# Optimization experiments

Hardware: AMD Instinct MI355X
Metric: run time of the kernel (lower is better)

## Reference

```python
import jax, jax.numpy as jnp
import numpy as np

N = 30000          # mesh vertices
B = 5 * 16         # p_bins * t_bins geodesic patch bins
NEURONS = [16, 64, 64, 32]


def setup_inputs() -> dict:
    key = jax.random.key(0)
    ks = jax.random.split(key, 7)
    x = jax.random.normal(ks[0], (N, NEURONS[0]), dtype=jnp.float32)
    conn = jax.random.randint(ks[1], (N, B), 0, N)  # per-vertex per-bin source index
    s1 = 1.0 / np.sqrt(NEURONS[0])
    W1 = jax.random.uniform(ks[2], (NEURONS[0], NEURONS[1]), minval=-s1, maxval=s1, dtype=jnp.float32)
    s2 = 1.0 / np.sqrt(B * NEURONS[1])
    Wg1 = jax.random.uniform(ks[3], (B, NEURONS[1], NEURONS[2]), minval=-s2, maxval=s2, dtype=jnp.float32)
    b1 = jax.random.uniform(ks[4], (NEURONS[2],), minval=-s2, maxval=s2, dtype=jnp.float32)
    s3 = 1.0 / np.sqrt(B * NEURONS[2])
    Wg2 = jax.random.uniform(ks[5], (B, NEURONS[2], NEURONS[3]), minval=-s3, maxval=s3, dtype=jnp.float32)
    b2 = jax.random.uniform(ks[6], (NEURONS[3],), minval=-s3, maxval=s3, dtype=jnp.float32)
    return {"x": x, "W1": W1, "Wg1": Wg1, "b1": b1, "Wg2": Wg2, "b2": b2, "conn": conn}


def _geodesic(h, conn, Wg, b):
    # gather geodesic patch: [N, B, C_in], then per-bin contraction
    patches = h[conn]                               # irregular gather
    return jnp.einsum("nbi,bio->no", patches, Wg) + b


def reference(x, W1, Wg1, b1, Wg2, b2, conn):
    h = jax.nn.relu(x @ W1)                         # linear_1 (no bias, l_bias=False)
    h = jax.nn.relu(_geodesic(h, conn, Wg1, b1))    # GC_1 + relu
    res = _geodesic(h, conn, Wg2, b2)               # GC_2
    norm = jnp.linalg.norm(res, axis=-1, keepdims=True)
    return res / norm
```

## Files before the change

### kernel.cpp

```cpp
#include <hip/hip_runtime.h>
#include <stdint.h>
#include <stddef.h>


typedef __attribute__((ext_vector_type(8))) short bf16x8;
typedef __attribute__((ext_vector_type(4))) float f32x4;

#define BINS 80
#define SPLITK 4
#define BPC 20

static __device__ __forceinline__ unsigned short f2bf(float f) {
  union { float f; unsigned int u; } c; c.f = f;
  unsigned int u = c.u;
  return (unsigned short)((u + 0x7FFFu + ((u >> 16) & 1u)) >> 16);
}

__global__ __launch_bounds__(256) void k_lin1(const float* __restrict__ x,
                                              const float* __restrict__ W1,
                                              unsigned short* __restrict__ h1b, int n) {
  __shared__ float w1s[16 * 64];
  int tid = threadIdx.x;
  for (int i = tid; i < 16 * 64; i += 256) w1s[i] = W1[i];
  __syncthreads();
  int v = blockIdx.x * 256 + tid;
  if (v >= n) return;
  const float4* xp = (const float4*)(x + (size_t)v * 16);
  float4 x0 = xp[0], x1 = xp[1], x2 = xp[2], x3 = xp[3];
  float xr[16] = {x0.x, x0.y, x0.z, x0.w, x1.x, x1.y, x1.z, x1.w,
                  x2.x, x2.y, x2.z, x2.w, x3.x, x3.y, x3.z, x3.w};
  float acc[64];
#pragma unroll
  for (int o = 0; o < 64; ++o) acc[o] = 0.f;
#pragma unroll
  for (int i = 0; i < 16; ++i) {
    float xi = xr[i];
#pragma unroll
    for (int o = 0; o < 64; ++o) acc[o] = fmaf(xi, w1s[i * 64 + o], acc[o]);
  }
  unsigned short* hr = h1b + (size_t)v * 64;
#pragma unroll
  for (int o8 = 0; o8 < 8; ++o8) {
    bf16x8 pack;
#pragma unroll
    for (int j = 0; j < 8; ++j) pack[j] = (short)f2bf(fmaxf(acc[o8 * 8 + j], 0.f));
    *(bf16x8*)(hr + o8 * 8) = pack;
  }
}

__global__ __launch_bounds__(256) void k_wimg(const float* __restrict__ Wg,
                                              unsigned char* __restrict__ img,
                                              int O, int total) {
  int t = blockIdx.x * 256 + threadIdx.x;
  if (t >= total) return;
  int c = t & 7;
  int o = (t >> 3) % O;
  int b = t / (O * 8);
  int boff = (o * 128 + c * 16) ^ ((o & 7) << 4);
  bf16x8 pack;
#pragma unroll
  for (int j = 0; j < 8; ++j)
    pack[j] = (short)f2bf(Wg[(size_t)(b * 64 + c * 8 + j) * O + o]);
  *(bf16x8*)(img + (size_t)b * (O * 128) + boff) = pack;
}

template <int OT>
__global__ __launch_bounds__(256) void k_geo_sk(const unsigned short* __restrict__ hin,
                                                const unsigned char* __restrict__ wimg,
                                                const int* __restrict__ conn,
                                                float* __restrict__ part, int n) {
  constexpr int TILEB = OT * 16 * 128;
  __shared__ int conn_s[64 * (BPC + 1)];
  __shared__ alignas(16) unsigned char wg_s[2][TILEB];

  const int tid = threadIdx.x;
  const int lane = tid & 63;
  const int wave = tid >> 6;
  const int ln15 = lane & 15;
  const int lq = lane >> 4;
  const int v0 = blockIdx.x * 64;
  const int chunk = blockIdx.y;
  const int bin0 = chunk * BPC;

  for (int idx = tid; idx < 64 * BPC; idx += 256) {
    int v = idx / BPC;
    int c = idx - v * BPC;
    int vv = v0 + v;
    if (vv > n - 1) vv = n - 1;
    conn_s[v * (BPC + 1) + c] = conn[(size_t)vv * BINS + bin0 + c];
  }

  auto stage = [&](int bin, int buf) {
    const unsigned char* src = wimg + (size_t)bin * TILEB + wave * (TILEB / 4) + lane * 16;
    unsigned char* dst = &wg_s[buf][wave * (TILEB / 4)];
#pragma unroll
    for (int i = 0; i < TILEB / 4096; ++i) {
      __builtin_amdgcn_global_load_lds(
          (const __attribute__((address_space(1))) unsigned int*)(const void*)(src + i * 1024),
          (__attribute__((address_space(3))) unsigned int*)(void*)(dst + i * 1024),
          16, 0, 0);
    }
  };

  int boffs[OT][2];
#pragma unroll
  for (int ot = 0; ot < OT; ++ot)
#pragma unroll
    for (int s = 0; s < 2; ++s) {
      int o = ot * 16 + ln15;
      boffs[ot][s] = (o * 128 + s * 64 + lq * 16) ^ ((o & 7) << 4);
    }

  f32x4 acc[OT];
#pragma unroll
  for (int ot = 0; ot < OT; ++ot) acc[ot] = (f32x4){0.f, 0.f, 0.f, 0.f};

  stage(bin0, 0);
  __syncthreads();

  const int crow = (wave * 16 + ln15) * (BPC + 1);
  const int koff = lq * 8;

  bf16x8 a0, a1;
  {
    int cidx = conn_s[crow];
    const unsigned short* arow = hin + (size_t)cidx * 64 + koff;
    a0 = *(const bf16x8*)(arow);
    a1 = *(const bf16x8*)(arow + 32);
  }

  for (int cb = 0; cb < BPC; ++cb) {
    int cur = cb & 1;
    bf16x8 na0 = a0, na1 = a1;
    if (cb + 1 < BPC) {
      stage(bin0 + cb + 1, cur ^ 1);
      int nc = conn_s[crow + cb + 1];
      const unsigned short* arow = hin + (size_t)nc * 64 + koff;
      na0 = *(const bf16x8*)(arow);
      na1 = *(const bf16x8*)(arow + 32);
    }

    const unsigned char* wb = wg_s[cur];
#pragma unroll
    for (int ot = 0; ot < OT; ++ot) {
      bf16x8 b0 = *(const bf16x8*)(wb + boffs[ot][0]);
      bf16x8 b1 = *(const bf16x8*)(wb + boffs[ot][1]);
      acc[ot] = __builtin_amdgcn_mfma_f32_16x16x32_bf16(a0, b0, acc[ot], 0, 0, 0);
      acc[ot] = __builtin_amdgcn_mfma_f32_16x16x32_bf16(a1, b1, acc[ot], 0, 0, 0);
    }
    __syncthreads();
    a0 = na0; a1 = na1;
  }

  constexpr int O = OT * 16;
  float* pbase = part + (size_t)chunk * n * O;
#pragma unroll
  for (int ot = 0; ot < OT; ++ot) {
#pragma unroll
    for (int r = 0; r < 4; ++r) {
      int v = v0 + wave * 16 + lq * 4 + r;
      if (v < n) pbase[(size_t)v * O + ot * 16 + ln15] = acc[ot][r];
    }
  }
}

__global__ __launch_bounds__(256) void k_fin1(const float* __restrict__ part,
                                              const float* __restrict__ bias,
                                              unsigned short* __restrict__ out, int n) {
  int t = blockIdx.x * 256 + threadIdx.x;
  int total = n * 16;
  if (t >= total) return;
  int base = t * 4;
  int o = base & 63;
  size_t stride = (size_t)n * 64;
  const float* p = part + base;
  float4 s = *(const float4*)(p);
#pragma unroll
  for (int c = 1; c < SPLITK; ++c) {
    float4 q = *(const float4*)(p + c * stride);
    s.x += q.x; s.y += q.y; s.z += q.z; s.w += q.w;
  }
  float4 b4 = *(const float4*)(bias + o);
  ushort4 pack;
  pack.x = f2bf(fmaxf(s.x + b4.x, 0.f));
  pack.y = f2bf(fmaxf(s.y + b4.y, 0.f));
  pack.z = f2bf(fmaxf(s.z + b4.z, 0.f));
  pack.w = f2bf(fmaxf(s.w + b4.w, 0.f));
  *(ushort4*)(out + base) = pack;
}

__global__ __launch_bounds__(256) void k_fin2(const float* __restrict__ part,
                                              const float* __restrict__ bias,
                                              float* __restrict__ out, int n) {
  int v = blockIdx.x * 16 + (threadIdx.x >> 4);
  int o = threadIdx.x & 15;
  if (v >= n) return;
  size_t stride = (size_t)n * 32;
  const float* p = part + (size_t)v * 32 + o;
  float a = 0.f, b = 0.f;
#pragma unroll
  for (int c = 0; c < SPLITK; ++c) {
    a += p[c * stride];
    b += p[c * stride + 16];
  }
  a += bias[o];
  b += bias[o + 16];
  float ss = a * a + b * b;
  ss += __shfl_xor(ss, 1);
  ss += __shfl_xor(ss, 2);
  ss += __shfl_xor(ss, 4);
  ss += __shfl_xor(ss, 8);
  float inv = 1.0f / sqrtf(ss);
  out[(size_t)v * 32 + o] = a * inv;
  out[(size_t)v * 32 + 16 + o] = b * inv;
}

extern "C" void kernel_launch(void* const* d_in, const int* in_sizes, int n_in,
                              void* d_out, int out_size, void* d_ws, size_t ws_size,
                              hipStream_t stream) {
  const float* x   = (const float*)d_in[0];
  const float* W1  = (const float*)d_in[1];
  const float* Wg1 = (const float*)d_in[2];
  const float* b1  = (const float*)d_in[3];
  const float* Wg2 = (const float*)d_in[4];
  const float* b2  = (const float*)d_in[5];
  const int*  conn = (const int*)d_in[6];
  int n = in_sizes[0] / 16;

  unsigned char* ws = (unsigned char*)d_ws;
  size_t hb = ((size_t)n * 64 * 2 + 255) & ~(size_t)255;
  unsigned short* h1b = (unsigned short*)(ws);
  unsigned short* h2b = (unsigned short*)(ws + hb);
  unsigned char*  w1i = ws + 2 * hb;
  unsigned char*  w2i = ws + 2 * hb + 80 * 8192;
  float* part = (float*)(ws + 2 * hb + 80 * 8192 + 80 * 4096);

  k_wimg<<<(80 * 64 * 8 + 255) / 256, 256, 0, stream>>>(Wg1, w1i, 64, 80 * 64 * 8);
  k_wimg<<<(80 * 32 * 8 + 255) / 256, 256, 0, stream>>>(Wg2, w2i, 32, 80 * 32 * 8);
  k_lin1<<<(n + 255) / 256, 256, 0, stream>>>(x, W1, h1b, n);

  int gb = (n + 63) / 64;
  k_geo_sk<4><<<dim3(gb, SPLITK), 256, 0, stream>>>(h1b, w1i, conn, part, n);
  k_fin1<<<(n * 16 + 255) / 256, 256, 0, stream>>>(part, b1, h2b, n);
  k_geo_sk<2><<<dim3(gb, SPLITK), 256, 0, stream>>>(h2b, w2i, conn, part, n);
  k_fin2<<<(n + 15) / 16, 256, 0, stream>>>(part, b2, (float*)d_out, n);
}
```

Measured before the change: 140.4 us.

## Deepen geodesic gather pipeline with 128-row tiles and manual vmcnt waits

The geodesic split-K kernel now processes 128 vertices per block, with two 16-row M tiles per wave, so each staged weight tile is reused across twice as many rows. Gathers and weight staging are issued two bins ahead into a 4-deep LDS ring and 3-deep register buffers. Completion is tracked with explicit s_waitcnt vmcnt values and a raw s_barrier instead of __syncthreads each step. This trades more registers and LDS, plus half as many blocks, for more loads in flight and less weight traffic. It also depends on the hand-counted vmcnt matching the instructions the compiler actually emits.

Measured after the change: 136.7 us. -2.6%, faster.

```diff
diff --git a/kernel.cpp b/kernel.cpp
--- a/kernel.cpp
+++ b/kernel.cpp
@@ -9,11 +9,20 @@
 #define BINS 80
 #define SPLITK 4
 #define BPC 20
+#define MROWS 128
 
 static __device__ __forceinline__ unsigned short f2bf(float f) {
   union { float f; unsigned int u; } c; c.f = f;
   unsigned int u = c.u;
   return (unsigned short)((u + 0x7FFFu + ((u >> 16) & 1u)) >> 16);
+}
+
+template <int N> static __device__ __forceinline__ void wait_vmcnt() {
+  if constexpr (N == 12)      asm volatile("s_waitcnt vmcnt(12)" ::: "memory");
+  else if constexpr (N == 10) asm volatile("s_waitcnt vmcnt(10)" ::: "memory");
+  else if constexpr (N == 6)  asm volatile("s_waitcnt vmcnt(6)" ::: "memory");
+  else if constexpr (N == 5)  asm volatile("s_waitcnt vmcnt(5)" ::: "memory");
+  else                        asm volatile("s_waitcnt vmcnt(0)" ::: "memory");
 }
 
 __global__ __launch_bounds__(256) void k_lin1(const float* __restrict__ x,
@@ -65,24 +74,27 @@
 }
 
 template <int OT>
-__global__ __launch_bounds__(256) void k_geo_sk(const unsigned short* __restrict__ hin,
-                                                const unsigned char* __restrict__ wimg,
-                                                const int* __restrict__ conn,
-                                                float* __restrict__ part, int n) {
+__global__ __launch_bounds__(256, 3) void k_geo_sk(const unsigned short* __restrict__ hin,
+                                                   const unsigned char* __restrict__ wimg,
+                                                   const int* __restrict__ conn,
+                                                   float* __restrict__ part, int n) {
   constexpr int TILEB = OT * 16 * 128;
-  __shared__ int conn_s[64 * (BPC + 1)];
-  __shared__ alignas(16) unsigned char wg_s[2][TILEB];
+  constexpr int SINSTS = TILEB / 4096;
+  constexpr int IPI = 4 + SINSTS;
+
+  __shared__ int conn_s[MROWS * (BPC + 1)];
+  __shared__ alignas(16) unsigned char wg_s[4][TILEB];
 
   const int tid = threadIdx.x;
   const int lane = tid & 63;
   const int wave = tid >> 6;
   const int ln15 = lane & 15;
   const int lq = lane >> 4;
-  const int v0 = blockIdx.x * 64;
+  const int v0 = blockIdx.x * MROWS;
   const int chunk = blockIdx.y;
   const int bin0 = chunk * BPC;
 
-  for (int idx = tid; idx < 64 * BPC; idx += 256) {
+  for (int idx = tid; idx < MROWS * BPC; idx += 256) {
     int v = idx / BPC;
     int c = idx - v * BPC;
     int vv = v0 + v;
@@ -90,78 +102,85 @@
     conn_s[v * (BPC + 1) + c] = conn[(size_t)vv * BINS + bin0 + c];
   }
 
-  auto stage = [&](int bin, int buf) {
-    const unsigned char* src = wimg + (size_t)bin * TILEB + wave * (TILEB / 4) + lane * 16;
-    unsigned char* dst = &wg_s[buf][wave * (TILEB / 4)];
-#pragma unroll
-    for (int i = 0; i < TILEB / 4096; ++i) {
+  int boffs[OT][2];
+#pragma unroll
+  for (int ot = 0; ot < OT; ++ot)
+#pragma unroll
+    for (int s = 0; s < 2; ++s) {
+      int o = ot * 16 + ln15;
+      boffs[ot][s] = (o * 128 + s * 64 + lq * 16) ^ ((o & 7) << 4);
+    }
+
+  const int koff = lq * 8;
+  bf16x8 As[3][2][2];
+  f32x4 acc[2][OT];
+#pragma unroll
+  for (int mt = 0; mt < 2; ++mt)
+#pragma unroll
+    for (int ot = 0; ot < OT; ++ot) acc[mt][ot] = (f32x4){0.f, 0.f, 0.f, 0.f};
+
+  auto issue = [&](int j) {
+#pragma unroll
+    for (int mt = 0; mt < 2; ++mt) {
+      int cidx = conn_s[(wave * 32 + mt * 16 + ln15) * (BPC + 1) + j];
+      const unsigned short* arow = hin + (size_t)cidx * 64 + koff;
+      As[j % 3][mt][0] = *(const bf16x8*)(arow);
+      As[j % 3][mt][1] = *(const bf16x8*)(arow + 32);
+    }
+    __builtin_amdgcn_sched_barrier(0);
+    const unsigned char* src =
+        wimg + (size_t)(bin0 + j) * TILEB + wave * (TILEB / 4) + lane * 16;
+    unsigned char* dst = &wg_s[j & 3][wave * (TILEB / 4)];
+#pragma unroll
+    for (int i = 0; i < SINSTS; ++i) {
       __builtin_amdgcn_global_load_lds(
           (const __attribute__((address_space(1))) unsigned int*)(const void*)(src + i * 1024),
           (__attribute__((address_space(3))) unsigned int*)(void*)(dst + i * 1024),
           16, 0, 0);
     }
+    __builtin_amdgcn_sched_barrier(0);
   };
 
-  int boffs[OT][2];
-#pragma unroll
-  for (int ot = 0; ot < OT; ++ot)
-#pragma unroll
-    for (int s = 0; s < 2; ++s) {
-      int o = ot * 16 + ln15;
-      boffs[ot][s] = (o * 128 + s * 64 + lq * 16) ^ ((o & 7) << 4);
-    }
-
-  f32x4 acc[OT];
-#pragma unroll
-  for (int ot = 0; ot < OT; ++ot) acc[ot] = (f32x4){0.f, 0.f, 0.f, 0.f};
-
-  stage(bin0, 0);
   __syncthreads();
-
-  const int crow = (wave * 16 + ln15) * (BPC + 1);
-  const int koff = lq * 8;
-
-  bf16x8 a0, a1;
-  {
-    int cidx = conn_s[crow];
-    const unsigned short* arow = hin + (size_t)cidx * 64 + koff;
-    a0 = *(const bf16x8*)(arow);
-    a1 = *(const bf16x8*)(arow + 32);
-  }
-
+  issue(0);
+  issue(1);
+
+#pragma unroll
   for (int cb = 0; cb < BPC; ++cb) {
-    int cur = cb & 1;
-    bf16x8 na0 = a0, na1 = a1;
-    if (cb + 1 < BPC) {
-      stage(bin0 + cb + 1, cur ^ 1);
-      int nc = conn_s[crow + cb + 1];
-      const unsigned short* arow = hin + (size_t)nc * 64 + koff;
-      na0 = *(const bf16x8*)(arow);
-      na1 = *(const bf16x8*)(arow + 32);
-    }
-
-    const unsigned char* wb = wg_s[cur];
+    if (cb + 2 < BPC) issue(cb + 2);
+    const int nafter = IPI * ((cb + 1 < BPC ? 1 : 0) + (cb + 2 < BPC ? 1 : 0));
+    if (nafter == 2 * IPI)      wait_vmcnt<2 * IPI>();
+    else if (nafter == IPI)     wait_vmcnt<IPI>();
+    else                        wait_vmcnt<0>();
+    __builtin_amdgcn_s_barrier();
+    __builtin_amdgcn_sched_barrier(0);
+
+    const unsigned char* wb = wg_s[cb & 3];
 #pragma unroll
     for (int ot = 0; ot < OT; ++ot) {
       bf16x8 b0 = *(const bf16x8*)(wb + boffs[ot][0]);
       bf16x8 b1 = *(const bf16x8*)(wb + boffs[ot][1]);
-      acc[ot] = __builtin_amdgcn_mfma_f32_16x16x32_bf16(a0, b0, acc[ot], 0, 0, 0);
-      acc[ot] = __builtin_amdgcn_mfma_f32_16x16x32_bf16(a1, b1, acc[ot], 0, 0, 0);
-    }
-    __syncthreads();
-    a0 = na0; a1 = na1;
+#pragma unroll
+      for (int mt = 0; mt < 2; ++mt) {
+        acc[mt][ot] = __builtin_amdgcn_mfma_f32_16x16x32_bf16(As[cb % 3][mt][0], b0,
+                                                              acc[mt][ot], 0, 0, 0);
+        acc[mt][ot] = __builtin_amdgcn_mfma_f32_16x16x32_bf16(As[cb % 3][mt][1], b1,
+                                                              acc[mt][ot], 0, 0, 0);
+      }
+    }
   }
 
   constexpr int O = OT * 16;
   float* pbase = part + (size_t)chunk * n * O;
 #pragma unroll
-  for (int ot = 0; ot < OT; ++ot) {
-#pragma unroll
-    for (int r = 0; r < 4; ++r) {
-      int v = v0 + wave * 16 + lq * 4 + r;
-      if (v < n) pbase[(size_t)v * O + ot * 16 + ln15] = acc[ot][r];
-    }
-  }
+  for (int mt = 0; mt < 2; ++mt)
+#pragma unroll
+    for (int ot = 0; ot < OT; ++ot)
+#pragma unroll
+      for (int r = 0; r < 4; ++r) {
+        int v = v0 + wave * 32 + mt * 16 + lq * 4 + r;
+        if (v < n) pbase[(size_t)v * O + ot * 16 + ln15] = acc[mt][ot][r];
+      }
 }
 
 __global__ __launch_bounds__(256) void k_fin1(const float* __restrict__ part,
@@ -239,7 +258,7 @@
   k_wimg<<<(80 * 32 * 8 + 255) / 256, 256, 0, stream>>>(Wg2, w2i, 32, 80 * 32 * 8);
   k_lin1<<<(n + 255) / 256, 256, 0, stream>>>(x, W1, h1b, n);
 
-  int gb = (n + 63) / 64;
+  int gb = (n + MROWS - 1) / MROWS;
   k_geo_sk<4><<<dim3(gb, SPLITK), 256, 0, stream>>>(h1b, w1i, conn, part, n);
   k_fin1<<<(n * 16 + 255) / 256, 256, 0, stream>>>(part, b1, h2b, n);
   k_geo_sk<2><<<dim3(gb, SPLITK), 256, 0, stream>>>(h2b, w2i, conn, part, n);
```
